# Kernel tuning notes

Measured on AMD Instinct MI355X. Metric: run time of the kernel, lower is better.

Reference implementation:

```python
import jax, jax.numpy as jnp
import numpy as np

T, B, D, H, E = 16, 4096, 256, 512, 32
EPS = 0.1

def setup_inputs() -> dict:
    key = jax.random.key(0)
    ks = jax.random.split(key, 8)
    return {
        "term_emb": jax.random.normal(ks[0], (T, B, D), dtype=jnp.float32),
        "pred_emb": jax.random.normal(ks[1], (E, B, D), dtype=jnp.float32),
        "inv_pred_emb": jax.random.normal(ks[2], (E, B, D), dtype=jnp.float32),
        "signs": jnp.ones((E,), dtype=jnp.float32),
        "W1": jax.random.normal(ks[3], (D, H), dtype=jnp.float32) * (1.0 / np.sqrt(D)),
        "b1": jnp.zeros((H,), dtype=jnp.float32),
        "W2": jax.random.normal(ks[4], (H, D), dtype=jnp.float32) * (1.0 / np.sqrt(H)),
        "b2": jnp.zeros((D,), dtype=jnp.float32),
        "heads": jax.random.randint(ks[5], (E,), 0, T, dtype=jnp.int64),
        "tails": jax.random.randint(ks[6], (E,), 0, T, dtype=jnp.int64),
    }

def reference(term_emb, pred_emb, inv_pred_emb, signs, W1, b1, W2, b2, heads, tails):
    # gather endpoint embeddings per edge: [E, B, D]
    h = term_emb[heads]
    t = term_emb[tails]
    s = signs[:, None, None]
    # estimate_tail_emb (TransE-style NBP): translate by relation embedding
    msg_to_tail = s * (h + pred_emb)      # message along edge direction
    msg_to_head = s * (t + inv_pred_emb)  # message along inverse direction
    # scatter-add messages into per-term slots (sum aggregation)
    agg = (jax.ops.segment_sum(msg_to_tail, tails, num_segments=T)
           + jax.ops.segment_sum(msg_to_head, heads, num_segments=T))
    agg = agg + EPS * term_emb  # residual with eps
    # 1-layer MLP: Linear -> ReLU -> Linear
    hidden = jax.nn.relu(jnp.einsum('tbd,dh->tbh', agg, W1) + b1)
    out = jnp.einsum('tbh,hd->tbd', hidden, W2) + b2
    return out
```

## Files before the change

kernel.cpp:

```cpp
#include <hip/hip_runtime.h>
#include <hip/hip_bf16.h>
#include <stdint.h>

#define T_DIM 16
#define B_DIM 4096
#define D_DIM 256
#define H_DIM 512
#define E_DIM 32
#define M_DIM (T_DIM * B_DIM)
#define BD_DIM (B_DIM * D_DIM)
#define EPS_F 0.1f

#define NSLICE 16
#define SH 32
#define HS_LD 40

typedef __attribute__((ext_vector_type(8))) short short8;
typedef __attribute__((ext_vector_type(4))) float f32x4;

#define GLOBAL_AS __attribute__((address_space(1)))
#define LDS_AS __attribute__((address_space(3)))

__device__ __forceinline__ uint32_t f2bf_rne(float x) {
  uint32_t u = __float_as_uint(x);
  return (u + 0x7fffu + ((u >> 16) & 1u)) >> 16;
}

__device__ __forceinline__ uint4 pack8(const float* f) {
  uint4 v;
  v.x = f2bf_rne(f[0]) | (f2bf_rne(f[1]) << 16);
  v.y = f2bf_rne(f[2]) | (f2bf_rne(f[3]) << 16);
  v.z = f2bf_rne(f[4]) | (f2bf_rne(f[5]) << 16);
  v.w = f2bf_rne(f[6]) | (f2bf_rne(f[7]) << 16);
  return v;
}

__global__ __launch_bounds__(256) void agg_prep_kernel(
    const float* __restrict__ term, const float* __restrict__ pred,
    const float* __restrict__ inv, const float* __restrict__ signs,
    const int* __restrict__ heads, const int* __restrict__ tails,
    const float* __restrict__ W1, const float* __restrict__ W2,
    uint16_t* __restrict__ agg, uint16_t* __restrict__ W1T, uint16_t* __restrict__ W2T) {
  if (blockIdx.y == T_DIM) {
    const int idx = blockIdx.x * 256 + threadIdx.x;
    const int d = idx >> 9, h = idx & (H_DIM - 1);
    W1T[h * D_DIM + d] = (uint16_t)f2bf_rne(W1[idx]);
    const int h2 = idx >> 8, d2 = idx & (D_DIM - 1);
    W2T[d2 * H_DIM + h2] = (uint16_t)f2bf_rne(W2[idx]);
    return;
  }

  __shared__ int sh_h[E_DIM], sh_t[E_DIM];
  __shared__ float sh_s[E_DIM];
  if (threadIdx.x < E_DIM) {
    int e = threadIdx.x;
    sh_h[e] = heads[e] & (T_DIM - 1);
    sh_t[e] = tails[e] & (T_DIM - 1);
    sh_s[e] = signs[e];
  }
  __syncthreads();

  const int t = blockIdx.y;
  const int j = (blockIdx.x * 256 + threadIdx.x) * 8;

  float acc[8];
  {
    f32x4 a = *reinterpret_cast<const f32x4*>(term + (size_t)t * BD_DIM + j);
    f32x4 b = *reinterpret_cast<const f32x4*>(term + (size_t)t * BD_DIM + j + 4);
    acc[0] = EPS_F * a[0]; acc[1] = EPS_F * a[1]; acc[2] = EPS_F * a[2]; acc[3] = EPS_F * a[3];
    acc[4] = EPS_F * b[0]; acc[5] = EPS_F * b[1]; acc[6] = EPS_F * b[2]; acc[7] = EPS_F * b[3];
  }

#pragma unroll 1
  for (int e = 0; e < E_DIM; ++e) {
    const float s = sh_s[e];
    if (sh_t[e] == t) {
      const f32x4* p = reinterpret_cast<const f32x4*>(pred + (size_t)e * BD_DIM + j);
      const float* hrow = term + (size_t)sh_h[e] * BD_DIM + j;
      f32x4 p0 = __builtin_nontemporal_load(p);
      f32x4 p1 = __builtin_nontemporal_load(p + 1);
      f32x4 h0 = *reinterpret_cast<const f32x4*>(hrow);
      f32x4 h1 = *reinterpret_cast<const f32x4*>(hrow + 4);
      acc[0] += s * (h0[0] + p0[0]); acc[1] += s * (h0[1] + p0[1]);
      acc[2] += s * (h0[2] + p0[2]); acc[3] += s * (h0[3] + p0[3]);
      acc[4] += s * (h1[0] + p1[0]); acc[5] += s * (h1[1] + p1[1]);
      acc[6] += s * (h1[2] + p1[2]); acc[7] += s * (h1[3] + p1[3]);
    }
    if (sh_h[e] == t) {
      const f32x4* iv = reinterpret_cast<const f32x4*>(inv + (size_t)e * BD_DIM + j);
      const float* trow = term + (size_t)sh_t[e] * BD_DIM + j;
      f32x4 i0 = __builtin_nontemporal_load(iv);
      f32x4 i1 = __builtin_nontemporal_load(iv + 1);
      f32x4 t0 = *reinterpret_cast<const f32x4*>(trow);
      f32x4 t1 = *reinterpret_cast<const f32x4*>(trow + 4);
      acc[0] += s * (t0[0] + i0[0]); acc[1] += s * (t0[1] + i0[1]);
      acc[2] += s * (t0[2] + i0[2]); acc[3] += s * (t0[3] + i0[3]);
      acc[4] += s * (t1[0] + i1[0]); acc[5] += s * (t1[1] + i1[1]);
      acc[6] += s * (t1[2] + i1[2]); acc[7] += s * (t1[3] + i1[3]);
    }
  }
  *reinterpret_cast<uint4*>(agg + (size_t)t * BD_DIM + j) = pack8(acc);
}

__global__ __launch_bounds__(256, 2) void mlp_fused(
    const uint16_t* __restrict__ A,
    const uint16_t* __restrict__ W1T,
    const uint16_t* __restrict__ W2T,
    const float* __restrict__ b1, const float* __restrict__ b2,
    float* __restrict__ Out) {
  __shared__ __align__(16) uint16_t As[64 * 256];
  __shared__ __align__(16) uint16_t Wb[2][SH * 256];
  __shared__ __align__(16) uint16_t Hs[64 * HS_LD];

  const int tid = threadIdx.x;
  const int w = tid >> 6;
  const int l = tid & 63;
  const int lane16 = l & 15;
  const int quad = l >> 4;
  const int m0 = blockIdx.x * 64;

  const int wm  = (w & 1) * 32;
  const int wnA = ((w >> 1) & 1) * 16;
  const int wn2 = ((w >> 1) & 1) * 128;

#pragma unroll
  for (int p = 0; p < 8; ++p) {
    const int off = p * 2048 + tid * 8;
    const int kc = off >> 11;
    const int row = (off >> 5) & 63;
    const int c = off & 31;
    const uint16_t* g = A + (size_t)(m0 + row) * D_DIM + kc * 32 + c;
    __builtin_amdgcn_global_load_lds((const GLOBAL_AS uint32_t*)g,
                                     (LDS_AS uint32_t*)(As + off), 16, 0, 0);
  }
#pragma unroll
  for (int p = 0; p < 4; ++p) {
    const int off = p * 2048 + tid * 8;
    const int kc = off >> 10;
    const int hl = (off >> 5) & 31;
    const int c = off & 31;
    const uint16_t* g = W1T + (size_t)hl * D_DIM + kc * 32 + c;
    __builtin_amdgcn_global_load_lds((const GLOBAL_AS uint32_t*)g,
                                     (LDS_AS uint32_t*)(Wb[0] + off), 16, 0, 0);
  }
  __syncthreads();

  f32x4 oacc[2][8];
#pragma unroll
  for (int i = 0; i < 2; ++i)
#pragma unroll
    for (int j = 0; j < 8; ++j) oacc[i][j] = (f32x4){0.f, 0.f, 0.f, 0.f};

  for (int s = 0; s < NSLICE; ++s) {
#pragma unroll
    for (int p = 0; p < 4; ++p) {
      const int off = p * 2048 + tid * 8;
      const int d = off >> 5;
      const int c = off & 31;
      const uint16_t* g = W2T + (size_t)d * H_DIM + s * SH + c;
      __builtin_amdgcn_global_load_lds((const GLOBAL_AS uint32_t*)g,
                                       (LDS_AS uint32_t*)(Wb[1] + off), 16, 0, 0);
    }

    f32x4 hacc[2];
#pragma unroll
    for (int i = 0; i < 2; ++i) hacc[i] = (f32x4){0.f, 0.f, 0.f, 0.f};

#pragma unroll
    for (int kk = 0; kk < 8; ++kk) {
      short8 af[2], bfr;
      bfr = *reinterpret_cast<const short8*>(Wb[0] + kk * 1024 + (wnA + lane16) * 32 + quad * 8);
#pragma unroll
      for (int i = 0; i < 2; ++i)
        af[i] = *reinterpret_cast<const short8*>(As + kk * 2048 + (wm + i * 16 + lane16) * 32 + quad * 8);
#pragma unroll
      for (int i = 0; i < 2; ++i)
        hacc[i] = __builtin_amdgcn_mfma_f32_16x16x32_bf16(af[i], bfr, hacc[i], 0, 0, 0);
    }

    {
      const int hloc = wnA + lane16;
      const float bv = b1[s * SH + hloc];
#pragma unroll
      for (int i = 0; i < 2; ++i) {
#pragma unroll
        for (int r = 0; r < 4; ++r) {
          const int row = wm + i * 16 + quad * 4 + r;
          const float x = fmaxf(hacc[i][r] + bv, 0.f);
          Hs[row * HS_LD + hloc] = (uint16_t)f2bf_rne(x);
        }
      }
    }
    __syncthreads();

    if (s < NSLICE - 1) {
#pragma unroll
      for (int p = 0; p < 4; ++p) {
        const int off = p * 2048 + tid * 8;
        const int kc = off >> 10;
        const int hl = (off >> 5) & 31;
        const int c = off & 31;
        const uint16_t* g = W1T + (size_t)((s + 1) * SH + hl) * D_DIM + kc * 32 + c;
        __builtin_amdgcn_global_load_lds((const GLOBAL_AS uint32_t*)g,
                                         (LDS_AS uint32_t*)(Wb[0] + off), 16, 0, 0);
      }
    }

    {
      short8 af2[2], bf2[8];
#pragma unroll
      for (int i = 0; i < 2; ++i)
        af2[i] = *reinterpret_cast<const short8*>(Hs + (wm + i * 16 + lane16) * HS_LD + quad * 8);
#pragma unroll
      for (int j = 0; j < 8; ++j)
        bf2[j] = *reinterpret_cast<const short8*>(Wb[1] + (wn2 + j * 16 + lane16) * 32 + quad * 8);
#pragma unroll
      for (int i = 0; i < 2; ++i)
#pragma unroll
        for (int j = 0; j < 8; ++j)
          oacc[i][j] = __builtin_amdgcn_mfma_f32_16x16x32_bf16(af2[i], bf2[j], oacc[i][j], 0, 0, 0);
    }
    __syncthreads();
  }

#pragma unroll
  for (int j = 0; j < 8; ++j) {
    const int col = wn2 + j * 16 + lane16;
    const float bv = b2[col];
#pragma unroll
    for (int i = 0; i < 2; ++i) {
#pragma unroll
      for (int r = 0; r < 4; ++r) {
        const int row = m0 + wm + i * 16 + quad * 4 + r;
        Out[(size_t)row * D_DIM + col] = oacc[i][j][r] + bv;
      }
    }
  }
}

extern "C" void kernel_launch(void* const* d_in, const int* in_sizes, int n_in,
                              void* d_out, int out_size, void* d_ws, size_t ws_size,
                              hipStream_t stream) {
  const float* term  = (const float*)d_in[0];
  const float* pred  = (const float*)d_in[1];
  const float* inv   = (const float*)d_in[2];
  const float* signs = (const float*)d_in[3];
  const float* W1    = (const float*)d_in[4];
  const float* b1    = (const float*)d_in[5];
  const float* W2    = (const float*)d_in[6];
  const float* b2    = (const float*)d_in[7];
  const int* heads   = (const int*)d_in[8];
  const int* tails   = (const int*)d_in[9];

  char* ws = (char*)d_ws;
  uint16_t* W1T = (uint16_t*)(ws);
  uint16_t* W2T = (uint16_t*)(ws + 262144);
  uint16_t* agg = (uint16_t*)(ws + 524288);

  agg_prep_kernel<<<dim3(BD_DIM / 8 / 256, T_DIM + 1), dim3(256), 0, stream>>>(
      term, pred, inv, signs, heads, tails, W1, W2, agg, W1T, W2T);
  mlp_fused<<<dim3(M_DIM / 64), dim3(256), 0, stream>>>(
      agg, W1T, W2T, b1, b2, (float*)d_out);
}
```

Baseline: 413.9 us.

## Fold term-embedding gathers into a 16x16 coefficient matrix per column

Reformulates the aggregation so each thread loads all 16 term rows for its columns once into registers and combines them through a 16x16 coefficient matrix (eps on the diagonal plus signed edge contributions) built in LDS with atomics. Each output term then only streams the per-edge pred/inv rows from per-term lists. This removes repeated global reads of term_emb (previously reloaded once per matching edge and per output term) and restructures the grid to one block per column chunk looping over all terms. The cost is much higher register pressure (32 f32x4 held live) and a serial per-term loop inside each thread.

```diff
diff --git a/kernel.cpp b/kernel.cpp
--- a/kernel.cpp
+++ b/kernel.cpp
@@ -14,6 +14,7 @@
 #define NSLICE 16
 #define SH 32
 #define HS_LD 40
+#define MAXS 64
 
 typedef __attribute__((ext_vector_type(8))) short short8;
 typedef __attribute__((ext_vector_type(4))) float f32x4;
@@ -35,14 +36,15 @@
   return v;
 }
 
-__global__ __launch_bounds__(256) void agg_prep_kernel(
+__global__ __launch_bounds__(256, 2) void agg_prep_kernel(
     const float* __restrict__ term, const float* __restrict__ pred,
     const float* __restrict__ inv, const float* __restrict__ signs,
     const int* __restrict__ heads, const int* __restrict__ tails,
     const float* __restrict__ W1, const float* __restrict__ W2,
     uint16_t* __restrict__ agg, uint16_t* __restrict__ W1T, uint16_t* __restrict__ W2T) {
-  if (blockIdx.y == T_DIM) {
-    const int idx = blockIdx.x * 256 + threadIdx.x;
+  const int tid = threadIdx.x;
+  if (blockIdx.x >= 512) {
+    const int idx = (blockIdx.x - 512) * 256 + tid;
     const int d = idx >> 9, h = idx & (H_DIM - 1);
     W1T[h * D_DIM + d] = (uint16_t)f2bf_rne(W1[idx]);
     const int h2 = idx >> 8, d2 = idx & (D_DIM - 1);
@@ -50,56 +52,73 @@
     return;
   }
 
-  __shared__ int sh_h[E_DIM], sh_t[E_DIM];
-  __shared__ float sh_s[E_DIM];
-  if (threadIdx.x < E_DIM) {
-    int e = threadIdx.x;
-    sh_h[e] = heads[e] & (T_DIM - 1);
-    sh_t[e] = tails[e] & (T_DIM - 1);
-    sh_s[e] = signs[e];
-  }
+  __shared__ float Cm[T_DIM][T_DIM];
+  __shared__ float Lsgn[T_DIM][MAXS];
+  __shared__ uint64_t Lptr[T_DIM][MAXS];
+  __shared__ int Lcnt[T_DIM];
+
+  Cm[tid >> 4][tid & 15] = ((tid >> 4) == (tid & 15)) ? EPS_F : 0.f;
+  if (tid < T_DIM) Lcnt[tid] = 0;
   __syncthreads();
-
-  const int t = blockIdx.y;
-  const int j = (blockIdx.x * 256 + threadIdx.x) * 8;
-
-  float acc[8];
-  {
-    f32x4 a = *reinterpret_cast<const f32x4*>(term + (size_t)t * BD_DIM + j);
-    f32x4 b = *reinterpret_cast<const f32x4*>(term + (size_t)t * BD_DIM + j + 4);
-    acc[0] = EPS_F * a[0]; acc[1] = EPS_F * a[1]; acc[2] = EPS_F * a[2]; acc[3] = EPS_F * a[3];
-    acc[4] = EPS_F * b[0]; acc[5] = EPS_F * b[1]; acc[6] = EPS_F * b[2]; acc[7] = EPS_F * b[3];
+  if (tid < E_DIM) {
+    const int e = tid;
+    const int hh = heads[e] & (T_DIM - 1);
+    const int tt = tails[e] & (T_DIM - 1);
+    const float s = signs[e];
+    atomicAdd(&Cm[tt][hh], s);
+    int i = atomicAdd(&Lcnt[tt], 1);
+    Lsgn[tt][i] = s; Lptr[tt][i] = (uint64_t)(pred + (size_t)e * BD_DIM);
+    atomicAdd(&Cm[hh][tt], s);
+    i = atomicAdd(&Lcnt[hh], 1);
+    Lsgn[hh][i] = s; Lptr[hh][i] = (uint64_t)(inv + (size_t)e * BD_DIM);
+  }
+  __syncthreads();
+
+  const int j = (blockIdx.x * 256 + tid) * 8;
+
+  f32x4 ta[T_DIM], tb[T_DIM];
+#pragma unroll
+  for (int s = 0; s < T_DIM; ++s) {
+    ta[s] = __builtin_nontemporal_load(reinterpret_cast<const f32x4*>(term + (size_t)s * BD_DIM + j));
+    tb[s] = __builtin_nontemporal_load(reinterpret_cast<const f32x4*>(term + (size_t)s * BD_DIM + j + 4));
   }
 
 #pragma unroll 1
-  for (int e = 0; e < E_DIM; ++e) {
-    const float s = sh_s[e];
-    if (sh_t[e] == t) {
-      const f32x4* p = reinterpret_cast<const f32x4*>(pred + (size_t)e * BD_DIM + j);
-      const float* hrow = term + (size_t)sh_h[e] * BD_DIM + j;
-      f32x4 p0 = __builtin_nontemporal_load(p);
-      f32x4 p1 = __builtin_nontemporal_load(p + 1);
-      f32x4 h0 = *reinterpret_cast<const f32x4*>(hrow);
-      f32x4 h1 = *reinterpret_cast<const f32x4*>(hrow + 4);
-      acc[0] += s * (h0[0] + p0[0]); acc[1] += s * (h0[1] + p0[1]);
-      acc[2] += s * (h0[2] + p0[2]); acc[3] += s * (h0[3] + p0[3]);
-      acc[4] += s * (h1[0] + p1[0]); acc[5] += s * (h1[1] + p1[1]);
-      acc[6] += s * (h1[2] + p1[2]); acc[7] += s * (h1[3] + p1[3]);
-    }
-    if (sh_h[e] == t) {
-      const f32x4* iv = reinterpret_cast<const f32x4*>(inv + (size_t)e * BD_DIM + j);
-      const float* trow = term + (size_t)sh_t[e] * BD_DIM + j;
-      f32x4 i0 = __builtin_nontemporal_load(iv);
-      f32x4 i1 = __builtin_nontemporal_load(iv + 1);
-      f32x4 t0 = *reinterpret_cast<const f32x4*>(trow);
-      f32x4 t1 = *reinterpret_cast<const f32x4*>(trow + 4);
-      acc[0] += s * (t0[0] + i0[0]); acc[1] += s * (t0[1] + i0[1]);
-      acc[2] += s * (t0[2] + i0[2]); acc[3] += s * (t0[3] + i0[3]);
-      acc[4] += s * (t1[0] + i1[0]); acc[5] += s * (t1[1] + i1[1]);
-      acc[6] += s * (t1[2] + i1[2]); acc[7] += s * (t1[3] + i1[3]);
-    }
-  }
-  *reinterpret_cast<uint4*>(agg + (size_t)t * BD_DIM + j) = pack8(acc);
+  for (int t = 0; t < T_DIM; ++t) {
+    f32x4 cv[4];
+#pragma unroll
+    for (int q = 0; q < 4; ++q)
+      cv[q] = *reinterpret_cast<const f32x4*>(&Cm[t][q * 4]);
+
+    float acc[8];
+#pragma unroll
+    for (int k = 0; k < 8; ++k) acc[k] = 0.f;
+
+#pragma unroll
+    for (int s = 0; s < T_DIM; ++s) {
+      const float cs = cv[s >> 2][s & 3];
+#pragma unroll
+      for (int k = 0; k < 4; ++k) {
+        acc[k]     += cs * ta[s][k];
+        acc[k + 4] += cs * tb[s][k];
+      }
+    }
+
+    const int n = Lcnt[t];
+#pragma unroll 2
+    for (int i = 0; i < n; ++i) {
+      const float sg = Lsgn[t][i];
+      const float* bp = (const float*)Lptr[t][i];
+      f32x4 p0 = __builtin_nontemporal_load(reinterpret_cast<const f32x4*>(bp + j));
+      f32x4 p1 = __builtin_nontemporal_load(reinterpret_cast<const f32x4*>(bp + j + 4));
+#pragma unroll
+      for (int k = 0; k < 4; ++k) {
+        acc[k]     += sg * p0[k];
+        acc[k + 4] += sg * p1[k];
+      }
+    }
+    *reinterpret_cast<uint4*>(agg + (size_t)t * BD_DIM + j) = pack8(acc);
+  }
 }
 
 __global__ __launch_bounds__(256, 2) void mlp_fused(
@@ -257,7 +276,7 @@
   uint16_t* W2T = (uint16_t*)(ws + 262144);
   uint16_t* agg = (uint16_t*)(ws + 524288);
 
-  agg_prep_kernel<<<dim3(BD_DIM / 8 / 256, T_DIM + 1), dim3(256), 0, stream>>>(
+  agg_prep_kernel<<<dim3(1024), dim3(256), 0, stream>>>(
       term, pred, inv, signs, heads, tails, W1, W2, agg, W1T, W2T);
   mlp_fused<<<dim3(M_DIM / 64), dim3(256), 0, stream>>>(
       agg, W1T, W2T, b1, b2, (float*)d_out);
```

Result: faster. 399.3 us (-3.5%).
